# Kernel optimization log

Measured on AMD Instinct MI355X. Metric: run time of the kernel, lower is better.

## Reference

```python
import jax, jax.numpy as jnp
import numpy as np

N_NODES = 100000
N_EDGES = 1600000
IN_CH = 128
HID = 128
OUT = 128


def gcn_conv(x, src, dst, dinv, W, b, n_nodes):
    """GCNConv with self-loops already folded into (src, dst, dinv).
    out[v] = sum_{(u->v)} dinv[u]*dinv[v] * (x @ W)[u] + b
    """
    xw = x @ W                                   # [N, F_out]
    norm = dinv[src] * dinv[dst]                 # [E+N]
    msg = xw[src] * norm[:, None]                # [E+N, F_out] (gather)
    out = jax.ops.segment_sum(msg, dst, num_segments=n_nodes)  # scatter-add
    return out + b


def setup_inputs() -> dict:
    key = jax.random.key(0)
    k = jax.random.split(key, 8)
    x = jax.random.normal(k[0], (N_NODES, IN_CH), dtype=jnp.float32)
    edge_index = jax.random.randint(k[1], (2, N_EDGES), 0, N_NODES, dtype=jnp.int64)
    s = 0.05
    W1 = jax.random.normal(k[2], (IN_CH, HID), dtype=jnp.float32) * s
    b1 = jnp.zeros((HID,), dtype=jnp.float32)
    W2 = jax.random.normal(k[3], (HID, HID), dtype=jnp.float32) * s
    b2 = jnp.zeros((HID,), dtype=jnp.float32)
    Wfc = jax.random.normal(k[4], (HID, OUT), dtype=jnp.float32) * s
    bfc = jnp.zeros((OUT,), dtype=jnp.float32)
    return {"x": x, "edge_index": edge_index, "W1": W1, "b1": b1,
            "W2": W2, "b2": b2, "Wfc": Wfc, "bfc": bfc}


def reference(x, edge_index, W1, b1, W2, b2, Wfc, bfc):
    n = x.shape[0]
    loop = jnp.arange(n, dtype=edge_index.dtype)
    src = jnp.concatenate([edge_index[0], loop])   # add self loops (PyG default)
    dst = jnp.concatenate([edge_index[1], loop])
    # symmetric normalization: deg over targets incl. self loops
    deg = jax.ops.segment_sum(jnp.ones_like(dst, dtype=x.dtype), dst, num_segments=n)
    dinv = jnp.where(deg > 0, jax.lax.rsqrt(deg), 0.0)
    h = jax.nn.relu(gcn_conv(x, src, dst, dinv, W1, b1, n))
    h = jax.nn.relu(gcn_conv(h, src, dst, dinv, W2, b2, n))
    pooled = jnp.mean(h, axis=0, keepdims=True)    # [1, HID]
    return pooled @ Wfc + bfc                      # [1, OUT]
```

## Files before the change

kernel.cpp:

```cpp
#include <hip/hip_runtime.h>
#include <stdint.h>

typedef unsigned short ushort_t;
typedef __attribute__((ext_vector_type(8))) short bf16x8;
typedef __attribute__((ext_vector_type(4))) float f32x4;
typedef __attribute__((ext_vector_type(2))) float f32x2;

#define BKT_SHIFT 7
#define BKT_W     128
#define NB_MAX    1024
#define KB_ITERS  16
#define KB_CHUNK  (256 * KB_ITERS)
#define BCAP      2560
#define PSLICES   8


__device__ __forceinline__ ushort_t f2bf(float f) {
    union { float f; uint32_t u; } a; a.f = f;
    uint32_t u = a.u;
    uint32_t r = (u + 0x7FFFu + ((u >> 16) & 1u)) >> 16;
    return (ushort_t)r;
}
__device__ __forceinline__ float bf_lo(uint32_t p) { return __uint_as_float(p << 16); }
__device__ __forceinline__ float bf_hi(uint32_t p) { return __uint_as_float(p & 0xFFFF0000u); }

__device__ __forceinline__ void bucket_scan(const int* __restrict__ cnts, int NB,
                                            int* pr, int* bb) {
    int t = threadIdx.x;
    int h[4];
    int sum = 0;
#pragma unroll
    for (int j = 0; j < 4; j++) {
        int idx = 4 * t + j;
        h[j] = (idx < NB) ? cnts[idx] : 0;
        sum += h[j];
    }
    pr[t] = sum;
    __syncthreads();
    for (int off = 1; off < 256; off <<= 1) {
        int x = (t >= off) ? pr[t - off] : 0;
        __syncthreads();
        pr[t] += x;
        __syncthreads();
    }
    int ex = pr[t] - sum;
#pragma unroll
    for (int j = 0; j < 4; j++) { bb[4 * t + j] = ex; ex += h[j]; }
    if (t == 255) bb[NB_MAX] = ex;
    __syncthreads();
}

__global__ __launch_bounds__(256) void kW_init(const float* __restrict__ W1,
                                               const float* __restrict__ W2,
                                               ushort_t* __restrict__ Wt1,
                                               ushort_t* __restrict__ Wt2,
                                               int* __restrict__ bcnt,
                                               float* __restrict__ pooled,
                                               int* __restrict__ counter) {
    int b = blockIdx.x, t = threadIdx.x;
    if (b < 64) {
        int i = b * 256 + t;
        int k = i >> 7, nn = i & 127;
        Wt1[nn * 128 + k] = f2bf(W1[i]);
        Wt2[nn * 128 + k] = f2bf(W2[i]);
    } else {
        for (int i = t; i < NB_MAX; i += 256) bcnt[i] = 0;
        for (int i = t; i < PSLICES * 128; i += 256) pooled[i] = 0.f;
        if (t == 0) *counter = 0;
    }
}

__global__ __launch_bounds__(256) void kB_bucket(const int* __restrict__ src,
                                                 const int* __restrict__ dst, int E, int NB,
                                                 int* __restrict__ bcnt,
                                                 uint32_t* __restrict__ bpack) {
    __shared__ int lh[NB_MAX];
    int t = threadIdx.x;
    for (int i = t; i < NB; i += 256) lh[i] = 0;
    __syncthreads();

    int base = blockIdx.x * KB_CHUNK;
    int dreg[KB_ITERS], rank[KB_ITERS];
#pragma unroll
    for (int i = 0; i < KB_ITERS; i++) {
        int e = base + t + i * 256;
        if (e < E) {
            int d = dst[e];
            dreg[i] = d;
            rank[i] = atomicAdd(&lh[d >> BKT_SHIFT], 1);
        } else {
            dreg[i] = -1; rank[i] = 0;
        }
    }
    __syncthreads();
    for (int i = t; i < NB; i += 256) {
        int c = lh[i];
        lh[i] = c ? atomicAdd(&bcnt[i], c) : 0;
    }
    __syncthreads();
#pragma unroll
    for (int i = 0; i < KB_ITERS; i++) {
        int e = base + t + i * 256;
        if (dreg[i] >= 0) {
            int d = dreg[i];
            int bkt = d >> BKT_SHIFT;
            size_t pos = (size_t)bkt * BCAP + lh[bkt] + rank[i];
            bpack[pos] = ((uint32_t)src[e] << BKT_SHIFT) | (uint32_t)(d & (BKT_W - 1));
        }
    }
}

__global__ __launch_bounds__(256) void kC_csr(const uint32_t* __restrict__ bpack,
                                              const int* __restrict__ bcnt, int NB, int n,
                                              float* __restrict__ dinv,
                                              int* __restrict__ offs,
                                              int* __restrict__ csr) {
    __shared__ int pr[256];
    __shared__ int bb[NB_MAX + 1];
    __shared__ int cnt[BKT_W];
    __shared__ int cur[BKT_W];

    const int t = threadIdx.x;
    const int b = blockIdx.x;
    bucket_scan(bcnt, NB, pr, bb);
    const int nb0 = b << BKT_SHIFT;
    const int wlen = min(BKT_W, n - nb0);
    const int e0 = bb[b];
    const int cntb = bb[b + 1] - e0;
    const uint32_t* bp = bpack + (size_t)b * BCAP;

    if (t < BKT_W) cnt[t] = 0;
    __syncthreads();
    for (int e = t; e < cntb; e += 256)
        atomicAdd(&cnt[bp[e] & (BKT_W - 1)], 1);
    __syncthreads();

    int v = (t < BKT_W) ? cnt[t] : 0;
    if (t < BKT_W) pr[t] = v;
    __syncthreads();
    for (int off = 1; off < BKT_W; off <<= 1) {
        int x = (t >= off && t < BKT_W) ? pr[t - off] : 0;
        __syncthreads();
        if (t < BKT_W) pr[t] += x;
        __syncthreads();
    }
    if (t < BKT_W) {
        int myoff = e0 + pr[t] - v;
        cur[t] = myoff;
        if (t < wlen) {
            offs[nb0 + t] = myoff;
            dinv[nb0 + t] = rsqrtf((float)(v + 1));
        }
    }
    if (b == NB - 1 && t == 0) offs[n] = bb[NB];
    __syncthreads();

    for (int e = t; e < cntb; e += 256) {
        uint32_t p = bp[e];
        int pos = atomicAdd(&cur[p & (BKT_W - 1)], 1);
        csr[pos] = (int)(p >> BKT_SHIFT);
    }
}

__global__ __launch_bounds__(256) void k_gemm1(const float* __restrict__ x,
                                               const ushort_t* __restrict__ Wt,
                                               const float* __restrict__ dinv,
                                               uint8_t* __restrict__ C, int n) {
    __shared__ ushort_t al[64 * 136];
    __shared__ ushort_t wl[128 * 136];
    const int t = threadIdx.x;
    const int l = t & 63;
    const int wave = t >> 6;
    const int lane15 = l & 15;
    const int quad = l >> 4;
    const int m0 = blockIdx.x * 64;
    const int rows = min(64, n - m0);

#pragma unroll
    for (int i = 0; i < 8; i++) {
        int f = t + 256 * i;
        int r = f >> 4, c = f & 15;
        *(uint4*)(&wl[r * 136 + c * 8]) = ((const uint4*)Wt)[f];
    }
    {
        const float4* Ap = (const float4*)(x + (size_t)m0 * 128);
        int nf = rows * 32;
#pragma unroll
        for (int i = 0; i < 8; i++) {
            int f = t + 256 * i;
            float4 vv = make_float4(0.f, 0.f, 0.f, 0.f);
            if (f < nf) vv = Ap[f];
            ushort4 us;
            us.x = f2bf(vv.x); us.y = f2bf(vv.y); us.z = f2bf(vv.z); us.w = f2bf(vv.w);
            int r = f >> 5, c = f & 31;
            *(ushort4*)(&al[r * 136 + c * 4]) = us;
        }
    }
    __syncthreads();

    f32x4 acc[8];
#pragma unroll
    for (int nt = 0; nt < 8; nt++) acc[nt] = (f32x4){0.f, 0.f, 0.f, 0.f};

    const int arow = wave * 16 + lane15;
#pragma unroll
    for (int kt = 0; kt < 4; kt++) {
        bf16x8 af = *(const bf16x8*)(&al[arow * 136 + kt * 32 + quad * 8]);
#pragma unroll
        for (int nt = 0; nt < 8; nt++) {
            bf16x8 bfr = *(const bf16x8*)(&wl[(nt * 16 + lane15) * 136 + kt * 32 + quad * 8]);
            acc[nt] = __builtin_amdgcn_mfma_f32_16x16x32_bf16(af, bfr, acc[nt], 0, 0, 0);
        }
    }

    const int rbase = m0 + wave * 16 + quad * 4;
    float dsc[4];
#pragma unroll
    for (int r = 0; r < 4; r++)
        dsc[r] = (rbase + r < n) ? dinv[rbase + r] : 0.f;
#pragma unroll
    for (int nt = 0; nt < 8; nt++) {
        int c0 = nt * 16 + lane15;
#pragma unroll
        for (int r = 0; r < 4; r += 2) {
            int pk = __builtin_amdgcn_cvt_pk_fp8_f32(acc[nt][r] * dsc[r],
                                                     acc[nt][r + 1] * dsc[r + 1], 0, false);
            int row0 = rbase + r, row1 = rbase + r + 1;
            if (row0 < n) C[(size_t)row0 * 128 + c0] = (uint8_t)pk;
            if (row1 < n) C[(size_t)row1 * 128 + c0] = (uint8_t)(pk >> 8);
        }
    }
}

__global__ __launch_bounds__(256) void k_gemm_mfma(const ushort_t* __restrict__ A,
                                                   const ushort_t* __restrict__ Wt,
                                                   const float* __restrict__ dinv,
                                                   uint8_t* __restrict__ C, int n) {
    __shared__ ushort_t al[64 * 136];
    __shared__ ushort_t wl[128 * 136];
    const int t = threadIdx.x;
    const int l = t & 63;
    const int wave = t >> 6;
    const int lane15 = l & 15;
    const int quad = l >> 4;
    const int m0 = blockIdx.x * 64;
    const int rows = min(64, n - m0);

#pragma unroll
    for (int i = 0; i < 8; i++) {
        int f = t + 256 * i;
        int r = f >> 4, c = f & 15;
        *(uint4*)(&wl[r * 136 + c * 8]) = ((const uint4*)Wt)[f];
    }
    {
        const uint4* Ap = (const uint4*)(A + (size_t)m0 * 128);
        int nf = rows * 16;
#pragma unroll
        for (int i = 0; i < 4; i++) {
            int f = t + 256 * i;
            uint4 v = make_uint4(0, 0, 0, 0);
            if (f < nf) v = Ap[f];
            int r = f >> 4, c = f & 15;
            *(uint4*)(&al[r * 136 + c * 8]) = v;
        }
    }
    __syncthreads();

    f32x4 acc[8];
#pragma unroll
    for (int nt = 0; nt < 8; nt++) acc[nt] = (f32x4){0.f, 0.f, 0.f, 0.f};

    const int arow = wave * 16 + lane15;
#pragma unroll
    for (int kt = 0; kt < 4; kt++) {
        bf16x8 af = *(const bf16x8*)(&al[arow * 136 + kt * 32 + quad * 8]);
#pragma unroll
        for (int nt = 0; nt < 8; nt++) {
            bf16x8 bfr = *(const bf16x8*)(&wl[(nt * 16 + lane15) * 136 + kt * 32 + quad * 8]);
            acc[nt] = __builtin_amdgcn_mfma_f32_16x16x32_bf16(af, bfr, acc[nt], 0, 0, 0);
        }
    }

    const int rbase = m0 + wave * 16 + quad * 4;
    float dsc[4];
#pragma unroll
    for (int r = 0; r < 4; r++)
        dsc[r] = (rbase + r < n) ? dinv[rbase + r] : 0.f;
#pragma unroll
    for (int nt = 0; nt < 8; nt++) {
        int c0 = nt * 16 + lane15;
#pragma unroll
        for (int r = 0; r < 4; r += 2) {
            int pk = __builtin_amdgcn_cvt_pk_fp8_f32(acc[nt][r] * dsc[r],
                                                     acc[nt][r + 1] * dsc[r + 1], 0, false);
            int row0 = rbase + r, row1 = rbase + r + 1;
            if (row0 < n) C[(size_t)row0 * 128 + c0] = (uint8_t)pk;
            if (row1 < n) C[(size_t)row1 * 128 + c0] = (uint8_t)(pk >> 8);
        }
    }
}

__global__ __launch_bounds__(256) void k_agg(const ushort_t* __restrict__ xw,
                                             const int* __restrict__ offsets,
                                             const int* __restrict__ csr,
                                             const float* __restrict__ dinv,
                                             const float* __restrict__ bias,
                                             ushort_t* __restrict__ out, int n) {
    const int l = threadIdx.x & 63;
    const int wave = (blockIdx.x << 2) | (threadIdx.x >> 6);
    const int wstride = gridDim.x << 2;
    const float2 bb = ((const float2*)bias)[l];
    uint32_t* out32 = (uint32_t*)out;

    for (int v = wave; v < n; v += wstride) {
        uint32_t pv = (uint32_t)xw[(size_t)v * 64 + l];
        f32x2 fs = __builtin_amdgcn_cvt_pk_f32_fp8((int)pv, false);
        float ax = fs.x, ay = fs.y;

        int e  = __builtin_amdgcn_readfirstlane(offsets[v]);
        int e1 = __builtin_amdgcn_readfirstlane(offsets[v + 1]);
        for (; e + 15 < e1; e += 16) {
            int u[16];
#pragma unroll
            for (int i = 0; i < 16; i++) u[i] = __builtin_amdgcn_readfirstlane(csr[e + i]);
            uint32_t p[16];
#pragma unroll
            for (int i = 0; i < 16; i++) p[i] = (uint32_t)xw[(size_t)u[i] * 64 + l];
#pragma unroll
            for (int i = 0; i < 16; i++) {
                f32x2 f = __builtin_amdgcn_cvt_pk_f32_fp8((int)p[i], false);
                ax += f.x; ay += f.y;
            }
        }
        for (; e + 7 < e1; e += 8) {
            int u[8];
#pragma unroll
            for (int i = 0; i < 8; i++) u[i] = __builtin_amdgcn_readfirstlane(csr[e + i]);
            uint32_t p[8];
#pragma unroll
            for (int i = 0; i < 8; i++) p[i] = (uint32_t)xw[(size_t)u[i] * 64 + l];
#pragma unroll
            for (int i = 0; i < 8; i++) {
                f32x2 f = __builtin_amdgcn_cvt_pk_f32_fp8((int)p[i], false);
                ax += f.x; ay += f.y;
            }
        }
        for (; e < e1; e++) {
            int u = __builtin_amdgcn_readfirstlane(csr[e]);
            uint32_t p = (uint32_t)xw[(size_t)u * 64 + l];
            f32x2 f = __builtin_amdgcn_cvt_pk_f32_fp8((int)p, false);
            ax += f.x; ay += f.y;
        }

        float dv = dinv[v];
        float ox = fmaxf(fmaf(ax, dv, bb.x), 0.f);
        float oy = fmaxf(fmaf(ay, dv, bb.y), 0.f);
        out32[(size_t)v * 64 + l] = ((uint32_t)f2bf(oy) << 16) | (uint32_t)f2bf(ox);
    }
}

__global__ __launch_bounds__(256) void k_poolfc(const ushort_t* __restrict__ h,
                                                float* __restrict__ pooled, int n,
                                                const float* __restrict__ Wfc,
                                                const float* __restrict__ bfc,
                                                float* __restrict__ out, float invN,
                                                int* __restrict__ counter) {
    __shared__ float red[512];
    __shared__ int lastFlag;
    __shared__ float pl[128];
    const int t = threadIdx.x;
    const int l = t & 63;
    const int wv = (blockIdx.x << 2) | (t >> 6);
    const int ws = gridDim.x << 2;
    const uint32_t* h32 = (const uint32_t*)h;

    const int span = (n + ws - 1) / ws;
    int r0 = wv * span;
    int r1 = min(n, r0 + span);
    float sx = 0.f, sy = 0.f;
    int r = r0;
    for (; r + 3 < r1; r += 4) {
        uint32_t p0 = h32[(size_t)r * 64 + l];
        uint32_t p1 = h32[(size_t)(r + 1) * 64 + l];
        uint32_t p2 = h32[(size_t)(r + 2) * 64 + l];
        uint32_t p3 = h32[(size_t)(r + 3) * 64 + l];
        sx += bf_lo(p0) + bf_lo(p1) + bf_lo(p2) + bf_lo(p3);
        sy += bf_hi(p0) + bf_hi(p1) + bf_hi(p2) + bf_hi(p3);
    }
    for (; r < r1; r++) {
        uint32_t p = h32[(size_t)r * 64 + l];
        sx += bf_lo(p); sy += bf_hi(p);
    }
    red[t] = sx;
    red[256 + t] = sy;
    __syncthreads();
    float* slice = pooled + (blockIdx.x & (PSLICES - 1)) * 128;
    if (t < 64) {
        sx = red[t] + red[t + 64] + red[t + 128] + red[t + 192];
        sy = red[256 + t] + red[256 + t + 64] + red[256 + t + 128] + red[256 + t + 192];
        atomicAdd(&slice[2 * l], sx);
        atomicAdd(&slice[2 * l + 1], sy);
    }
    __threadfence();
    __syncthreads();
    if (t == 0) {
        int old = atomicAdd(counter, 1);
        lastFlag = (old == (int)gridDim.x - 1);
    }
    __syncthreads();
    if (lastFlag) {
        if (t < 128) {
            float acc = 0.f;
#pragma unroll
            for (int s = 0; s < PSLICES; s++)
                acc += atomicAdd(&pooled[s * 128 + t], 0.f);
            pl[t] = acc;
        }
        __syncthreads();
        if (t < 128) {
            float acc = bfc[t];
#pragma unroll 8
            for (int k = 0; k < 128; k++)
                acc = fmaf(pl[k] * invN, Wfc[k * 128 + t], acc);
            out[t] = acc;
        }
    }
}

extern "C" void kernel_launch(void* const* d_in, const int* in_sizes, int n_in,
                              void* d_out, int out_size, void* d_ws, size_t ws_size,
                              hipStream_t stream) {
    const float* x    = (const float*)d_in[0];
    const int*   ei   = (const int*)d_in[1];
    const float* W1   = (const float*)d_in[2];
    const float* b1   = (const float*)d_in[3];
    const float* W2   = (const float*)d_in[4];
    const float* b2   = (const float*)d_in[5];
    const float* Wfc  = (const float*)d_in[6];
    const float* bfc  = (const float*)d_in[7];
    float*       out  = (float*)d_out;

    const int n = in_sizes[0] / 128;
    const int E = in_sizes[1] / 2;
    const int* src = ei;
    const int* dst = ei + E;
    const int NB = (n + BKT_W - 1) >> BKT_SHIFT;

    char* w = (char*)d_ws;
    uint8_t*  xwq = (uint8_t*)w;  w += (size_t)n * 128;
    ushort_t* h   = (ushort_t*)w; w += (size_t)n * 128 * sizeof(ushort_t);
    int*      csr = (int*)w;      w += (size_t)E * sizeof(int);
    uint32_t* bpack = (uint32_t*)w; w += (size_t)NB * BCAP * sizeof(uint32_t);
    float* dinv = (float*)w;  w += (size_t)n * sizeof(float);
    int*   offs = (int*)w;    w += (size_t)(n + 1) * sizeof(int);
    w = (char*)(((uintptr_t)w + 127) & ~(uintptr_t)127);
    int*   bcnt  = (int*)w;   w += NB_MAX * sizeof(int);
    int*   counter = (int*)w; w += 32 * sizeof(int);
    float* pooled = (float*)w; w += PSLICES * 128 * sizeof(float);
    ushort_t* Wt1 = (ushort_t*)w; w += 16384 * sizeof(ushort_t);
    ushort_t* Wt2 = (ushort_t*)w; w += 16384 * sizeof(ushort_t);

    const int ntiles64 = (n + 63) / 64;
    const float invN = 1.0f / (float)n;

    kW_init<<<65, 256, 0, stream>>>(W1, W2, Wt1, Wt2, bcnt, pooled, counter);
    kB_bucket<<<(E + KB_CHUNK - 1) / KB_CHUNK, 256, 0, stream>>>(src, dst, E, NB, bcnt, bpack);
    kC_csr<<<NB, 256, 0, stream>>>(bpack, bcnt, NB, n, dinv, offs, csr);
    k_gemm1<<<ntiles64, 256, 0, stream>>>(x, Wt1, dinv, xwq, n);

    k_agg<<<8192, 256, 0, stream>>>((const ushort_t*)xwq, offs, csr, dinv, b1, h, n);
    k_gemm_mfma<<<ntiles64, 256, 0, stream>>>(h, Wt2, dinv, xwq, n);
    k_agg<<<8192, 256, 0, stream>>>((const ushort_t*)xwq, offs, csr, dinv, b2, h, n);

    k_poolfc<<<256, 256, 0, stream>>>(h, pooled, n, Wfc, bfc, out, invN, counter);
}
```

Before: 296.2 us.

## Pad CSR rows to multiples of four with dummy zero node for vector index loads

Each destination's neighbour list is padded to a multiple of four entries, and the padding points to an extra all-zero row appended to the feature buffer. The CSR is laid out per bucket at a fixed stride, which removes the global bucket prefix scan from the CSR build. The aggregation kernel then reads neighbour indices with int4 loads and drops its scalar tail loop. The cost is extra gathers of the zero row for padding entries, a larger CSR buffer, and a fixed per-bucket capacity that could overflow on skewed graphs.

```diff
diff --git a/kernel.cpp b/kernel.cpp
--- a/kernel.cpp
+++ b/kernel.cpp
@@ -12,6 +12,7 @@
 #define KB_ITERS  16
 #define KB_CHUNK  (256 * KB_ITERS)
 #define BCAP      2560
+#define CSTRIDE   2944
 #define PSLICES   8
 
 
@@ -23,32 +24,6 @@
 }
 __device__ __forceinline__ float bf_lo(uint32_t p) { return __uint_as_float(p << 16); }
 __device__ __forceinline__ float bf_hi(uint32_t p) { return __uint_as_float(p & 0xFFFF0000u); }
-
-__device__ __forceinline__ void bucket_scan(const int* __restrict__ cnts, int NB,
-                                            int* pr, int* bb) {
-    int t = threadIdx.x;
-    int h[4];
-    int sum = 0;
-#pragma unroll
-    for (int j = 0; j < 4; j++) {
-        int idx = 4 * t + j;
-        h[j] = (idx < NB) ? cnts[idx] : 0;
-        sum += h[j];
-    }
-    pr[t] = sum;
-    __syncthreads();
-    for (int off = 1; off < 256; off <<= 1) {
-        int x = (t >= off) ? pr[t - off] : 0;
-        __syncthreads();
-        pr[t] += x;
-        __syncthreads();
-    }
-    int ex = pr[t] - sum;
-#pragma unroll
-    for (int j = 0; j < 4; j++) { bb[4 * t + j] = ex; ex += h[j]; }
-    if (t == 255) bb[NB_MAX] = ex;
-    __syncthreads();
-}
 
 __global__ __launch_bounds__(256) void kW_init(const float* __restrict__ W1,
                                                const float* __restrict__ W2,
@@ -56,7 +31,8 @@
                                                ushort_t* __restrict__ Wt2,
                                                int* __restrict__ bcnt,
                                                float* __restrict__ pooled,
-                                               int* __restrict__ counter) {
+                                               int* __restrict__ counter,
+                                               uint8_t* __restrict__ xwq, int n) {
     int b = blockIdx.x, t = threadIdx.x;
     if (b < 64) {
         int i = b * 256 + t;
@@ -66,6 +42,7 @@
     } else {
         for (int i = t; i < NB_MAX; i += 256) bcnt[i] = 0;
         for (int i = t; i < PSLICES * 128; i += 256) pooled[i] = 0.f;
+        if (t < 32) ((uint32_t*)(xwq + (size_t)n * 128))[t] = 0u;
         if (t == 0) *counter = 0;
     }
 }
@@ -114,20 +91,20 @@
                                               const int* __restrict__ bcnt, int NB, int n,
                                               float* __restrict__ dinv,
                                               int* __restrict__ offs,
+                                              int* __restrict__ ends,
                                               int* __restrict__ csr) {
-    __shared__ int pr[256];
-    __shared__ int bb[NB_MAX + 1];
+    __shared__ int pr[BKT_W];
     __shared__ int cnt[BKT_W];
     __shared__ int cur[BKT_W];
+    __shared__ int pend[BKT_W];
 
     const int t = threadIdx.x;
     const int b = blockIdx.x;
-    bucket_scan(bcnt, NB, pr, bb);
     const int nb0 = b << BKT_SHIFT;
     const int wlen = min(BKT_W, n - nb0);
-    const int e0 = bb[b];
-    const int cntb = bb[b + 1] - e0;
+    const int cntb = bcnt[b];
     const uint32_t* bp = bpack + (size_t)b * BCAP;
+    const int base = b * CSTRIDE;
 
     if (t < BKT_W) cnt[t] = 0;
     __syncthreads();
@@ -136,7 +113,8 @@
     __syncthreads();
 
     int v = (t < BKT_W) ? cnt[t] : 0;
-    if (t < BKT_W) pr[t] = v;
+    int pv = (v + 3) & ~3;
+    if (t < BKT_W) pr[t] = pv;
     __syncthreads();
     for (int off = 1; off < BKT_W; off <<= 1) {
         int x = (t >= off && t < BKT_W) ? pr[t - off] : 0;
@@ -145,20 +123,26 @@
         __syncthreads();
     }
     if (t < BKT_W) {
-        int myoff = e0 + pr[t] - v;
-        cur[t] = myoff;
+        int st = base + pr[t] - pv;
+        cur[t] = st;
+        pend[t] = st + pv;
         if (t < wlen) {
-            offs[nb0 + t] = myoff;
+            offs[nb0 + t] = st;
+            ends[nb0 + t] = st + pv;
             dinv[nb0 + t] = rsqrtf((float)(v + 1));
         }
     }
-    if (b == NB - 1 && t == 0) offs[n] = bb[NB];
     __syncthreads();
 
     for (int e = t; e < cntb; e += 256) {
         uint32_t p = bp[e];
         int pos = atomicAdd(&cur[p & (BKT_W - 1)], 1);
         csr[pos] = (int)(p >> BKT_SHIFT);
+    }
+    __syncthreads();
+    if (t < BKT_W) {
+        int qe = pend[t];
+        for (int q = cur[t]; q < qe; q++) csr[q] = n;
     }
 }
 
@@ -302,6 +286,7 @@
 
 __global__ __launch_bounds__(256) void k_agg(const ushort_t* __restrict__ xw,
                                              const int* __restrict__ offsets,
+                                             const int* __restrict__ ends,
                                              const int* __restrict__ csr,
                                              const float* __restrict__ dinv,
                                              const float* __restrict__ bias,
@@ -318,11 +303,28 @@
         float ax = fs.x, ay = fs.y;
 
         int e  = __builtin_amdgcn_readfirstlane(offsets[v]);
-        int e1 = __builtin_amdgcn_readfirstlane(offsets[v + 1]);
+        int e1 = __builtin_amdgcn_readfirstlane(ends[v]);
+
         for (; e + 15 < e1; e += 16) {
+            const int4* c4 = (const int4*)(csr + e);
+            int4 w0 = c4[0], w1 = c4[1], w2 = c4[2], w3 = c4[3];
             int u[16];
-#pragma unroll
-            for (int i = 0; i < 16; i++) u[i] = __builtin_amdgcn_readfirstlane(csr[e + i]);
+            u[0]  = __builtin_amdgcn_readfirstlane(w0.x);
+            u[1]  = __builtin_amdgcn_readfirstlane(w0.y);
+            u[2]  = __builtin_amdgcn_readfirstlane(w0.z);
+            u[3]  = __builtin_amdgcn_readfirstlane(w0.w);
+            u[4]  = __builtin_amdgcn_readfirstlane(w1.x);
+            u[5]  = __builtin_amdgcn_readfirstlane(w1.y);
+            u[6]  = __builtin_amdgcn_readfirstlane(w1.z);
+            u[7]  = __builtin_amdgcn_readfirstlane(w1.w);
+            u[8]  = __builtin_amdgcn_readfirstlane(w2.x);
+            u[9]  = __builtin_amdgcn_readfirstlane(w2.y);
+            u[10] = __builtin_amdgcn_readfirstlane(w2.z);
+            u[11] = __builtin_amdgcn_readfirstlane(w2.w);
+            u[12] = __builtin_amdgcn_readfirstlane(w3.x);
+            u[13] = __builtin_amdgcn_readfirstlane(w3.y);
+            u[14] = __builtin_amdgcn_readfirstlane(w3.z);
+            u[15] = __builtin_amdgcn_readfirstlane(w3.w);
             uint32_t p[16];
 #pragma unroll
             for (int i = 0; i < 16; i++) p[i] = (uint32_t)xw[(size_t)u[i] * 64 + l];
@@ -333,9 +335,17 @@
             }
         }
         for (; e + 7 < e1; e += 8) {
+            const int4* c4 = (const int4*)(csr + e);
+            int4 w0 = c4[0], w1 = c4[1];
             int u[8];
-#pragma unroll
-            for (int i = 0; i < 8; i++) u[i] = __builtin_amdgcn_readfirstlane(csr[e + i]);
+            u[0] = __builtin_amdgcn_readfirstlane(w0.x);
+            u[1] = __builtin_amdgcn_readfirstlane(w0.y);
+            u[2] = __builtin_amdgcn_readfirstlane(w0.z);
+            u[3] = __builtin_amdgcn_readfirstlane(w0.w);
+            u[4] = __builtin_amdgcn_readfirstlane(w1.x);
+            u[5] = __builtin_amdgcn_readfirstlane(w1.y);
+            u[6] = __builtin_amdgcn_readfirstlane(w1.z);
+            u[7] = __builtin_amdgcn_readfirstlane(w1.w);
             uint32_t p[8];
 #pragma unroll
             for (int i = 0; i < 8; i++) p[i] = (uint32_t)xw[(size_t)u[i] * 64 + l];
@@ -345,11 +355,21 @@
                 ax += f.x; ay += f.y;
             }
         }
-        for (; e < e1; e++) {
-            int u = __builtin_amdgcn_readfirstlane(csr[e]);
-            uint32_t p = (uint32_t)xw[(size_t)u * 64 + l];
-            f32x2 f = __builtin_amdgcn_cvt_pk_f32_fp8((int)p, false);
-            ax += f.x; ay += f.y;
+        for (; e + 3 < e1; e += 4) {
+            int4 w0 = *(const int4*)(csr + e);
+            int u[4];
+            u[0] = __builtin_amdgcn_readfirstlane(w0.x);
+            u[1] = __builtin_amdgcn_readfirstlane(w0.y);
+            u[2] = __builtin_amdgcn_readfirstlane(w0.z);
+            u[3] = __builtin_amdgcn_readfirstlane(w0.w);
+            uint32_t p[4];
+#pragma unroll
+            for (int i = 0; i < 4; i++) p[i] = (uint32_t)xw[(size_t)u[i] * 64 + l];
+#pragma unroll
+            for (int i = 0; i < 4; i++) {
+                f32x2 f = __builtin_amdgcn_cvt_pk_f32_fp8((int)p[i], false);
+                ax += f.x; ay += f.y;
+            }
         }
 
         float dv = dinv[v];
@@ -447,12 +467,13 @@
     const int NB = (n + BKT_W - 1) >> BKT_SHIFT;
 
     char* w = (char*)d_ws;
-    uint8_t*  xwq = (uint8_t*)w;  w += (size_t)n * 128;
+    uint8_t*  xwq = (uint8_t*)w;  w += (size_t)(n + 1) * 128;
     ushort_t* h   = (ushort_t*)w; w += (size_t)n * 128 * sizeof(ushort_t);
-    int*      csr = (int*)w;      w += (size_t)E * sizeof(int);
+    int*      csr = (int*)w;      w += (size_t)NB * CSTRIDE * sizeof(int);
     uint32_t* bpack = (uint32_t*)w; w += (size_t)NB * BCAP * sizeof(uint32_t);
     float* dinv = (float*)w;  w += (size_t)n * sizeof(float);
-    int*   offs = (int*)w;    w += (size_t)(n + 1) * sizeof(int);
+    int*   offs = (int*)w;    w += (size_t)n * sizeof(int);
+    int*   ends = (int*)w;    w += (size_t)n * sizeof(int);
     w = (char*)(((uintptr_t)w + 127) & ~(uintptr_t)127);
     int*   bcnt  = (int*)w;   w += NB_MAX * sizeof(int);
     int*   counter = (int*)w; w += 32 * sizeof(int);
@@ -463,14 +484,14 @@
     const int ntiles64 = (n + 63) / 64;
     const float invN = 1.0f / (float)n;
 
-    kW_init<<<65, 256, 0, stream>>>(W1, W2, Wt1, Wt2, bcnt, pooled, counter);
+    kW_init<<<65, 256, 0, stream>>>(W1, W2, Wt1, Wt2, bcnt, pooled, counter, xwq, n);
     kB_bucket<<<(E + KB_CHUNK - 1) / KB_CHUNK, 256, 0, stream>>>(src, dst, E, NB, bcnt, bpack);
-    kC_csr<<<NB, 256, 0, stream>>>(bpack, bcnt, NB, n, dinv, offs, csr);
+    kC_csr<<<NB, 256, 0, stream>>>(bpack, bcnt, NB, n, dinv, offs, ends, csr);
     k_gemm1<<<ntiles64, 256, 0, stream>>>(x, Wt1, dinv, xwq, n);
 
-    k_agg<<<8192, 256, 0, stream>>>((const ushort_t*)xwq, offs, csr, dinv, b1, h, n);
+    k_agg<<<8192, 256, 0, stream>>>((const ushort_t*)xwq, offs, ends, csr, dinv, b1, h, n);
     k_gemm_mfma<<<ntiles64, 256, 0, stream>>>(h, Wt2, dinv, xwq, n);
-    k_agg<<<8192, 256, 0, stream>>>((const ushort_t*)xwq, offs, csr, dinv, b2, h, n);
+    k_agg<<<8192, 256, 0, stream>>>((const ushort_t*)xwq, offs, ends, csr, dinv, b2, h, n);
 
     k_poolfc<<<256, 256, 0, stream>>>(h, pooled, n, Wfc, bfc, out, invN, counter);
 }
```

Result: faster. 272.0 us (-8.2%).
